# Performance work log

Measured on AMD Instinct MI355X. Metric: run time of the kernel, lower is better.

Reference implementation:

```python
import jax, jax.numpy as jnp
import numpy as np

MX_D, MN_D, CENTERS, WIDTH, SLOPE = 10.0, 0.0, 16, 1.0, 0.01
T_STEPS = 3


def _lrelu(x):
    return jax.nn.leaky_relu(x, SLOPE)


def _gauss(d):
    # d: [B,E,1] distances -> [B,E,CENTERS] gaussian radial basis
    mu = jnp.linspace(MN_D, MX_D, CENTERS, dtype=d.dtype)
    return jnp.exp(-jnp.square((d - mu[None, None, :]) / WIDTH))


def _equiv_message(v, idx2, n_recv, W1, W2, b, aw, ab):
    # v: [B,E,F] = concat(sender feats, receiver feats, bond feats).
    # Outer-product expand over receiver-cell axis (einsum with one-hot),
    # permutation-equivariant linear (local term + cell-sum term), LeakyReLU,
    # gather receiver cell, sigmoid attention gate, scatter_add to receivers.
    B, E, _ = v.shape
    O = W1.shape[1]
    oh = jax.nn.one_hot(idx2, n_recv, dtype=v.dtype)                 # [E,N]
    y_loc = jnp.einsum('bef,fo->beo', v, W1)                          # per-cell term
    y_sum = jnp.einsum('bef,fo->beo', v, W2) + b                      # cell-sum term (sum_n v*oh = v)
    y = _lrelu(y_loc[..., None] * oh[None, :, None, :] + y_sum[..., None])  # [B,E,O,N]
    gidx = jnp.broadcast_to(idx2[None, :, None, None], (B, E, O, 1))
    lat = jnp.take_along_axis(y, gidx, axis=3)[..., 0]                # [B,E,O]
    lat = jax.nn.sigmoid(lat @ aw + ab[None, None, :]) * lat          # attention gating
    return jnp.zeros((B, n_recv, O), v.dtype).at[:, idx2].add(lat)    # scatter_add over receivers


def _forward(sites, bonds, sites_p, bonds_sp, bonds_ps,
             se_W, se_b, sep_W, sep_b, ee_W, ee_b, eep_W, eep_b,
             eq_W1_ss, eq_W2_ss, eq_b_ss, att_w_ss, att_b_ss,
             eq_W1_ps, eq_W2_ps, eq_b_ps, att_w_ps, att_b_ps,
             eq_W1_sp, eq_W2_sp, eq_b_sp, att_w_sp, att_b_sp,
             nu_W1, nu_b1, nu_W2, nu_b2, nup_W1, nup_b1, nup_W2, nup_b2,
             p1_W, p1_b, p2a_W, p2a_b, p2b_W, p2b_b, p3_W, p3_b,
             idx1, idx2, idx1_sp, idx2_sp, idx1_ps, idx2_ps):
    s = _lrelu(sites @ se_W + se_b)          # [B,N,D] site embedding
    sp = _lrelu(sites_p @ sep_W + sep_b)     # [B,Np,D] pore embedding
    be = _lrelu(_gauss(bonds) @ ee_W + ee_b)
    bsp = _lrelu(_gauss(bonds_sp) @ eep_W + eep_b)
    bps = _lrelu(_gauss(bonds_ps) @ eep_W + eep_b)
    N, Np = s.shape[1], sp.shape[1]
    for t in range(T_STEPS):  # fixed number of message-passing layers
        v_ss = jnp.concatenate([s[:, idx1], s[:, idx2], be], -1)
        m = _equiv_message(v_ss, idx2, N, eq_W1_ss[t], eq_W2_ss[t], eq_b_ss[t], att_w_ss[t], att_b_ss[t])
        v_ps = jnp.concatenate([sp[:, idx1_ps], s[:, idx2_ps], bps], -1)
        m_ps = _equiv_message(v_ps, idx2_ps, N, eq_W1_ps[t], eq_W2_ps[t], eq_b_ps[t], att_w_ps[t], att_b_ps[t])
        v_sp = jnp.concatenate([s[:, idx1_sp], sp[:, idx2_sp], bsp], -1)
        m_sp = _equiv_message(v_sp, idx2_sp, Np, eq_W1_sp[t], eq_W2_sp[t], eq_b_sp[t], att_w_sp[t], att_b_sp[t])
        h = jnp.concatenate([s, m, m_ps], -1)
        h = _lrelu(_lrelu(h @ nu_W1[t] + nu_b1[t]) @ nu_W2[t] + nu_b2[t])
        s = s + h                              # residual node update (sites)
        hp = jnp.concatenate([sp, m_sp], -1)
        hp = _lrelu(_lrelu(hp @ nup_W1[t] + nup_b1[t]) @ nup_W2[t] + nup_b2[t])
        sp = sp + hp                           # residual node update (pores)
    x = _lrelu(s @ p1_W + p1_b).sum(1)        # sum pool over sites
    x = _lrelu(x @ p2a_W + p2a_b)
    x = _lrelu(x @ p2b_W + p2b_b)
    return x @ p3_W + p3_b                    # [B, out_size]


def setup_inputs():
    key = jax.random.key(0)
    ks = iter(jax.random.split(key, 80))
    B, N, Np, E, Esp = 4, 128, 16, 1280, 1024
    D, C, O, M, T = 32, CENTERS, 32, 64, T_STEPS
    Fin = 2 * D + 16  # sender + receiver + edge embedding

    def nrm(shape, fan):
        return jax.random.normal(next(ks), shape, jnp.float32) / np.float32(np.sqrt(fan))

    inp = {}
    inp['sites'] = jax.random.uniform(next(ks), (B, N, 1), jnp.float32)
    inp['bonds'] = jax.random.uniform(next(ks), (B, E, 1), jnp.float32) * MX_D
    inp['sites_p'] = jax.random.uniform(next(ks), (B, Np, 2), jnp.float32)
    inp['bonds_sp'] = jax.random.uniform(next(ks), (B, Esp, 1), jnp.float32) * MX_D
    inp['bonds_ps'] = jax.random.uniform(next(ks), (B, Esp, 1), jnp.float32) * MX_D
    inp['idx1'] = jax.random.randint(next(ks), (E,), 0, N, jnp.int32)
    inp['idx2'] = jax.random.randint(next(ks), (E,), 0, N, jnp.int32)
    inp['idx1_sp'] = jax.random.randint(next(ks), (Esp,), 0, N, jnp.int32)
    inp['idx2_sp'] = jax.random.randint(next(ks), (Esp,), 0, Np, jnp.int32)
    inp['idx1_ps'] = jax.random.randint(next(ks), (Esp,), 0, Np, jnp.int32)
    inp['idx2_ps'] = jax.random.randint(next(ks), (Esp,), 0, N, jnp.int32)
    # embeddings
    inp['se_W'] = nrm((1, D), 1); inp['se_b'] = nrm((D,), D)
    inp['sep_W'] = nrm((2, D), 2); inp['sep_b'] = nrm((D,), D)
    inp['ee_W'] = nrm((C, 16), C); inp['ee_b'] = nrm((16,), 16)
    inp['eep_W'] = nrm((C, 16), C); inp['eep_b'] = nrm((16,), 16)
    # equivariant message layers (stacked over T steps)
    for suf in ('ss', 'ps', 'sp'):
        inp['eq_W1_' + suf] = nrm((T, Fin, O), Fin)
        inp['eq_W2_' + suf] = nrm((T, Fin, O), Fin)
        inp['eq_b_' + suf] = nrm((T, O), O)
        inp['att_w_' + suf] = nrm((T, O, 1), O)
        inp['att_b_' + suf] = nrm((T, 1), 1)
    # node updates: sites take 2 message streams, pores take 1
    inp['nu_W1'] = nrm((T, D + 2 * O, D), D + 2 * O); inp['nu_b1'] = nrm((T, D), D)
    inp['nu_W2'] = nrm((T, D, D), D); inp['nu_b2'] = nrm((T, D), D)
    inp['nup_W1'] = nrm((T, D + O, D), D + O); inp['nup_b1'] = nrm((T, D), D)
    inp['nup_W2'] = nrm((T, D, D), D); inp['nup_b2'] = nrm((T, D), D)
    # prediction head
    inp['p1_W'] = nrm((D, M), D); inp['p1_b'] = nrm((M,), M)
    inp['p2a_W'] = nrm((M, M), M); inp['p2a_b'] = nrm((M,), M)
    inp['p2b_W'] = nrm((M, M), M); inp['p2b_b'] = nrm((M,), M)
    inp['p3_W'] = nrm((M, 1), M); inp['p3_b'] = nrm((1,), 1)
    return inp


def reference(sites, bonds, sites_p, bonds_sp, bonds_ps,
              se_W, se_b, sep_W, sep_b, ee_W, ee_b, eep_W, eep_b,
              eq_W1_ss, eq_W2_ss, eq_b_ss, att_w_ss, att_b_ss,
              eq_W1_ps, eq_W2_ps, eq_b_ps, att_w_ps, att_b_ps,
              eq_W1_sp, eq_W2_sp, eq_b_sp, att_w_sp, att_b_sp,
              nu_W1, nu_b1, nu_W2, nu_b2, nup_W1, nup_b1, nup_W2, nup_b2,
              p1_W, p1_b, p2a_W, p2a_b, p2b_W, p2b_b, p3_W, p3_b,
              idx1, idx2, idx1_sp, idx2_sp, idx1_ps, idx2_ps):
    return _forward(sites, bonds, sites_p, bonds_sp, bonds_ps,
                    se_W, se_b, sep_W, sep_b, ee_W, ee_b, eep_W, eep_b,
                    eq_W1_ss, eq_W2_ss, eq_b_ss, att_w_ss, att_b_ss,
                    eq_W1_ps, eq_W2_ps, eq_b_ps, att_w_ps, att_b_ps,
                    eq_W1_sp, eq_W2_sp, eq_b_sp, att_w_sp, att_b_sp,
                    nu_W1, nu_b1, nu_W2, nu_b2, nup_W1, nup_b1, nup_W2, nup_b2,
                    p1_W, p1_b, p2a_W, p2a_b, p2b_W, p2b_b, p3_W, p3_b,
                    idx1, idx2, idx1_sp, idx2_sp, idx1_ps, idx2_ps)
```

## Files before the change

kernel.cpp:

```cpp
#include <hip/hip_runtime.h>
#include <math.h>

#define BB   4
#define NN   128
#define NPP  16
#define EEE  1280
#define ESP  1024
#define DD   32
#define CC   16
#define OO   32
#define FIN  80
#define MMM  64
#define TT   3
#define TPB  256
#define SPB  512

#define MAXDEG_SS 48
#define MAXDEG_SP 192

constexpr int OFF_S    = 0;
constexpr int OFF_SP   = OFF_S   + BB*NN*DD;
constexpr int OFF_BE   = OFF_SP  + BB*NPP*DD;
constexpr int OFF_BSP  = OFF_BE  + BB*EEE*CC;
constexpr int OFF_BPS  = OFF_BSP + BB*ESP*CC;
constexpr int OFF_PRJ  = OFF_BPS + BB*ESP*CC;
constexpr int P_SASS = 0;
constexpr int P_SBSS = P_SASS + BB*NN*OO;
constexpr int P_SBPS = P_SBSS + BB*NN*OO;
constexpr int P_SASP = P_SBPS + BB*NN*OO;
constexpr int P_PAPS = P_SASP + BB*NN*OO;
constexpr int P_PBSP = P_PAPS + BB*NPP*OO;
constexpr int PRJ_SZ = P_PBSP + BB*NPP*OO;
constexpr int OFF_POOL = OFF_PRJ + 2*PRJ_SZ;
constexpr int OFF_CSR  = OFF_POOL + BB*MMM;
constexpr int SS_CNT  = 0;
constexpr int PS_CNT  = SS_CNT + NN;
constexpr int SP_CNT  = PS_CNT + NN;
constexpr int TICKET  = SP_CNT + NPP;
constexpr int SS_PAIR = 274;
constexpr int PS_PAIR = SS_PAIR + NN*MAXDEG_SS*2;
constexpr int SP_PAIR = PS_PAIR + NN*MAXDEG_SS*2;

__device__ __forceinline__ float lrelu(float x) { return x > 0.f ? x : 0.01f * x; }

__device__ __forceinline__ float dot16r(const float* ef, const float* we) {
    float4 f0 = *(const float4*)(ef);
    float4 f1 = *(const float4*)(ef + 4);
    float4 f2 = *(const float4*)(ef + 8);
    float4 f3 = *(const float4*)(ef + 12);
    return f0.x*we[ 0] + f0.y*we[ 1] + f0.z*we[ 2] + f0.w*we[ 3]
         + f1.x*we[ 4] + f1.y*we[ 5] + f1.z*we[ 6] + f1.w*we[ 7]
         + f2.x*we[ 8] + f2.y*we[ 9] + f2.z*we[10] + f2.w*we[11]
         + f3.x*we[12] + f3.y*we[13] + f3.z*we[14] + f3.w*we[15];
}

__device__ __forceinline__ float red32(float r) {
#pragma unroll
    for (int mm = 16; mm > 0; mm >>= 1) r += __shfl_xor(r, mm, 32);
    return r;
}

__device__ __forceinline__ void edge_embed(float d, const float* W, const float* bvec, float* out) {
    float g[CC];
#pragma unroll
    for (int c = 0; c < CC; ++c) {
        float mu = (10.0f / 15.0f) * (float)c;
        float z = d - mu;
        g[c] = expf(-z * z);
    }
#pragma unroll
    for (int j = 0; j < CC; ++j) {
        float a = bvec[j];
#pragma unroll
        for (int c = 0; c < CC; ++c) a += g[c] * W[c * CC + j];
        out[j] = lrelu(a);
    }
}

__device__ __forceinline__ void csr_wave(const int* recv, const int* send, int E, int r,
                                         int* cnt, int2* pair, int maxdeg, int lane) {
    int base = 0;
    for (int c = 0; c < E; c += 64) {
        const int e = c + lane;
        const bool m = (recv[e] == r);
        const unsigned long long mask = __ballot(m);
        if (m) {
            const int pos = base + __popcll(mask & ((1ull << lane) - 1ull));
            if (pos < maxdeg) pair[pos] = make_int2(e, send[e]);
        }
        base += (int)__popcll(mask);
    }
    if (lane == 0) cnt[r] = base < maxdeg ? base : maxdeg;
}

__global__ __launch_bounds__(TPB) void k_init(
    const float* sites, const float* bonds, const float* sites_p,
    const float* bonds_sp, const float* bonds_ps,
    const int* idx1, const int* idx2, const int* idx1_ps, const int* idx2_ps,
    const int* idx1_sp, const int* idx2_sp,
    const float* se_W, const float* se_b, const float* sep_W, const float* sep_b,
    const float* ee_W, const float* ee_b, const float* eep_W, const float* eep_b,
    const float* eqW1_ss, const float* eqW2_ss,
    const float* eqW1_ps, const float* eqW2_ps,
    const float* eqW1_sp, const float* eqW2_sp,
    float* ws)
{
    __shared__ float smem[4416];
    const int blk = blockIdx.x;
    const int tid = threadIdx.x;
    int* csr = (int*)(ws + OFF_CSR);

    if (blk == 0 && tid == 0) csr[TICKET] = 0;

    if (blk < 253) {
        const int totalA = BB*MMM + BB*EEE + BB*ESP + BB*ESP;
        for (int i = blk*TPB + tid; i < totalA; i += 253*TPB) {
            int r = i;
            if (r < BB*MMM) { ws[OFF_POOL + r] = 0.f; continue; }
            r -= BB*MMM;
            if (r < BB*EEE) { edge_embed(bonds[r],    ee_W,  ee_b,  ws + OFF_BE  + r*CC); continue; }
            r -= BB*EEE;
            if (r < BB*ESP) { edge_embed(bonds_sp[r], eep_W, eep_b, ws + OFF_BSP + r*CC); continue; }
            r -= BB*ESP;
            edge_embed(bonds_ps[r], eep_W, eep_b, ws + OFF_BPS + r*CC);
        }
    }
    if (blk < 72) {
        float* prj0 = ws + OFF_PRJ;
        const int el = tid >> 5, o = tid & 31;
        float* sP   = smem;
        float* sRow = smem + 4160;
        if (blk < 64) {
            const int g = blk*8 + el;
            float x = sites[g];
            float v0 = lrelu(x * se_W[o] + se_b[o]);
            ws[OFF_S + g*DD + o] = v0;
            sRow[el*32 + o] = v0;
            for (int i2 = tid; i2 < 4096; i2 += TPB) {
                int m = i2 >> 10, j = i2 & 1023, d = j >> 5, oo = j & 31;
                int row = (m == 1 || m == 2) ? (DD + d) : d;
                float wv;
                if (m < 2)      wv = eqW1_ss[row*OO + oo] + eqW2_ss[row*OO + oo];
                else if (m==2)  wv = eqW1_ps[row*OO + oo] + eqW2_ps[row*OO + oo];
                else            wv = eqW1_sp[row*OO + oo] + eqW2_sp[row*OO + oo];
                sP[i2] = wv;
            }
            __syncthreads();
            float p0=0.f,p1=0.f,p2=0.f,p3=0.f;
#pragma unroll
            for (int d = 0; d < 32; ++d) {
                float sv = sRow[el*32 + d];
                p0 += sv * sP[        d*32 + o];
                p1 += sv * sP[1024 +  d*32 + o];
                p2 += sv * sP[2048 +  d*32 + o];
                p3 += sv * sP[3072 +  d*32 + o];
            }
            prj0[P_SASS + g*OO + o] = p0;
            prj0[P_SBSS + g*OO + o] = p1;
            prj0[P_SBPS + g*OO + o] = p2;
            prj0[P_SASP + g*OO + o] = p3;
        } else {
            const int g = (blk-64)*8 + el;
            float x0 = sites_p[g*2], x1 = sites_p[g*2+1];
            float v0 = lrelu(x0 * sep_W[o] + x1 * sep_W[DD + o] + sep_b[o]);
            ws[OFF_SP + g*DD + o] = v0;
            sRow[el*32 + o] = v0;
            for (int i2 = tid; i2 < 2048; i2 += TPB) {
                int m = i2 >> 10, j = i2 & 1023, d = j >> 5, oo = j & 31;
                int row = (m == 0) ? d : (DD + d);
                float wv;
                if (m == 0) wv = eqW1_ps[row*OO + oo] + eqW2_ps[row*OO + oo];
                else        wv = eqW1_sp[row*OO + oo] + eqW2_sp[row*OO + oo];
                sP[i2] = wv;
            }
            __syncthreads();
            float p0=0.f,p1=0.f;
#pragma unroll
            for (int d = 0; d < 32; ++d) {
                float sv = sRow[el*32 + d];
                p0 += sv * sP[        d*32 + o];
                p1 += sv * sP[1024 +  d*32 + o];
            }
            prj0[P_PAPS + g*OO + o] = p0;
            prj0[P_PBSP + g*OO + o] = p1;
        }
    }
    if (blk >= 72 && blk < 140) {
        const int widx = (blk - 72) * 4 + (tid >> 6);
        const int lane = tid & 63;
        if (widx < NN) {
            csr_wave(idx2, idx1, EEE, widx, csr + SS_CNT,
                     (int2*)(csr + SS_PAIR) + widx*MAXDEG_SS, MAXDEG_SS, lane);
        } else if (widx < 2*NN) {
            const int r = widx - NN;
            csr_wave(idx2_ps, idx1_ps, ESP, r, csr + PS_CNT,
                     (int2*)(csr + PS_PAIR) + r*MAXDEG_SS, MAXDEG_SS, lane);
        } else if (widx < 2*NN + NPP) {
            const int r = widx - 2*NN;
            csr_wave(idx2_sp, idx1_sp, ESP, r, csr + SP_CNT,
                     (int2*)(csr + SP_PAIR) + r*MAXDEG_SP, MAXDEG_SP, lane);
        }
    }
}

__global__ __launch_bounds__(SPB) void k_step(
    const float* eqW1_ss, const float* eqW2_ss, const float* eqb_ss, const float* aw_ss, const float* ab_ss,
    const float* eqW1_ps, const float* eqW2_ps, const float* eqb_ps, const float* aw_ps, const float* ab_ps,
    const float* eqW1_sp, const float* eqW2_sp, const float* eqb_sp, const float* aw_sp, const float* ab_sp,
    const float* nuW1, const float* nub1, const float* nuW2, const float* nub2,
    const float* nupW1, const float* nupb1, const float* nupW2, const float* nupb2,
    const float* p1W, const float* p1b,
    const float* p2aW, const float* p2ab, const float* p2bW, const float* p2bb,
    const float* p3W, const float* p3b,
    float* ws, float* out, int t)
{
    __shared__ float sRed[768];
    __shared__ float sH[96], sU[32], sSnew[32];
    __shared__ float sHy[256], sHz[256];
    __shared__ int sWin;
    const int tid = threadIdx.x, blk = blockIdx.x;
    const int slot = tid >> 5, o = tid & 31;
    const int par = t & 1;
    const float* PRJ  = ws + OFF_PRJ + par * PRJ_SZ;
    float*       PRJn = ws + OFF_PRJ + (par ^ 1) * PRJ_SZ;
    const int* csr = (const int*)(ws + OFF_CSR);

    if (blk < 512) {
        const int g = blk, b = g >> 7, n = g & 127;
        const bool is_ss = slot < 8;
        const int q = slot & 7;
        const float* w1p = is_ss ? eqW1_ss : eqW1_ps;
        const float* w2p = is_ss ? eqW2_ss : eqW2_ps;
        const float* wa = w1p + t*FIN*OO + 2*DD*OO + o;
        const float* wb = w2p + t*FIN*OO + 2*DD*OO + o;
        float we[16];
#pragma unroll
        for (int c = 0; c < 16; ++c) we[c] = wa[c*OO] + wb[c*OO];
        const float bias = (is_ss ? eqb_ss : eqb_ps)[t*OO + o];
        const float awo  = (is_ss ? aw_ss  : aw_ps )[t*OO + o];
        const float abv  = (is_ss ? ab_ss  : ab_ps )[t];
        const float sb   = PRJ[(is_ss ? P_SBSS : P_SBPS) + g*OO + o];
        const float* SAb = is_ss ? (PRJ + P_SASS + b*(NN*OO))
                                 : (PRJ + P_PAPS + b*(NPP*OO));
        const float* EFb = is_ss ? (ws + OFF_BE  + b*(EEE*CC))
                                 : (ws + OFF_BPS + b*(ESP*CC));
        const int cnt = is_ss ? csr[SS_CNT + n] : csr[PS_CNT + n];
        const int2* lst = is_ss ? ((const int2*)(csr + SS_PAIR) + n*MAXDEG_SS)
                                : ((const int2*)(csr + PS_PAIR) + n*MAXDEG_SS);
        float acc = 0.f;
        for (int k = q; k < cnt; k += 8) {
            const int2 es = lst[k];
            float a = bias + sb + SAb[es.y*OO + o] + dot16r(EFb + es.x*CC, we);
            float u = lrelu(a);
            float rr = red32(u * awo);
            acc += u / (1.f + expf(-(rr + abv)));
        }
        sRed[slot*32 + o] = acc;
        if (tid < 32) sH[tid] = ws[OFF_S + g*DD + tid];
        __syncthreads();
        if (tid < 64) {
            const int r2 = tid >> 5, oo = tid & 31;
            float mv = 0.f;
#pragma unroll
            for (int j = 0; j < 8; ++j) mv += sRed[(r2*8 + j)*32 + oo];
            sH[32 + r2*32 + oo] = mv;
        }
        __syncthreads();
        if (tid < 32) {
            const float* W1 = nuW1 + t*(96*32);
            float a = nub1[t*32 + tid];
#pragma unroll
            for (int f = 0; f < 96; ++f) a += sH[f] * W1[f*32 + tid];
            sU[tid] = lrelu(a);
        }
        __syncthreads();
        if (tid < 32) {
            const float* W2 = nuW2 + t*(32*32);
            float a = nub2[t*32 + tid];
#pragma unroll
            for (int k2 = 0; k2 < 32; ++k2) a += sU[k2] * W2[k2*32 + tid];
            const float snew = sH[tid] + lrelu(a);
            ws[OFF_S + g*DD + tid] = snew;
            sSnew[tid] = snew;
        }
        __syncthreads();
        if (t < TT-1) {
            if (tid < 128) {
                const int tn = t + 1;
                const int m = slot;
                const float *w1m, *w2m; float* dst;
                if (m == 0)      { w1m = eqW1_ss + tn*FIN*OO;         w2m = eqW2_ss + tn*FIN*OO;         dst = PRJn + P_SASS; }
                else if (m == 1) { w1m = eqW1_ss + tn*FIN*OO + DD*OO; w2m = eqW2_ss + tn*FIN*OO + DD*OO; dst = PRJn + P_SBSS; }
                else if (m == 2) { w1m = eqW1_ps + tn*FIN*OO + DD*OO; w2m = eqW2_ps + tn*FIN*OO + DD*OO; dst = PRJn + P_SBPS; }
                else             { w1m = eqW1_sp + tn*FIN*OO;         w2m = eqW2_sp + tn*FIN*OO;         dst = PRJn + P_SASP; }
                float a = 0.f;
#pragma unroll
                for (int d = 0; d < 32; ++d) a += sSnew[d] * (w1m[d*OO + o] + w2m[d*OO + o]);
                dst[g*OO + o] = a;
            }
        } else {
            if (tid < 64) {
                float a = p1b[tid];
#pragma unroll
                for (int d = 0; d < 32; ++d) a += sSnew[d] * p1W[d*MMM + tid];
                atomicAdd(&ws[OFF_POOL + b*MMM + tid], lrelu(a));
            }
            __syncthreads();
            if (tid == 0) {
                int* ticket = (int*)(ws + OFF_CSR) + TICKET;
                int p = __hip_atomic_fetch_add(ticket, 1, __ATOMIC_ACQ_REL, __HIP_MEMORY_SCOPE_AGENT);
                sWin = (p == 511) ? 1 : 0;
            }
            __syncthreads();
            if (sWin) {
                float* sx = sRed;
                if (tid < 256)
                    sx[tid] = __hip_atomic_load(&ws[OFF_POOL + tid], __ATOMIC_RELAXED, __HIP_MEMORY_SCOPE_AGENT);
                __syncthreads();
                if (tid < 256) {
                    const int b2 = tid >> 6, mm = tid & 63;
                    float a = p2ab[mm];
#pragma unroll
                    for (int k = 0; k < MMM; ++k) a += sx[b2*64 + k] * p2aW[k*MMM + mm];
                    sHy[tid] = lrelu(a);
                }
                __syncthreads();
                if (tid < 256) {
                    const int b2 = tid >> 6, mm = tid & 63;
                    float a = p2bb[mm];
#pragma unroll
                    for (int k = 0; k < MMM; ++k) a += sHy[b2*64 + k] * p2bW[k*MMM + mm];
                    sHz[tid] = lrelu(a);
                }
                __syncthreads();
                if (tid < BB) {
                    float acc2 = p3b[0];
#pragma unroll
                    for (int k = 0; k < MMM; ++k) acc2 += sHz[tid*64 + k] * p3W[k];
                    out[tid] = acc2;
                }
            }
        }
    } else {
        const int g = blk - 512, b = g >> 4, p = g & 15;
        const float* wa = eqW1_sp + t*FIN*OO + 2*DD*OO + o;
        const float* wb = eqW2_sp + t*FIN*OO + 2*DD*OO + o;
        float we[16];
#pragma unroll
        for (int c = 0; c < 16; ++c) we[c] = wa[c*OO] + wb[c*OO];
        const float bias = eqb_sp[t*OO + o];
        const float awo  = aw_sp[t*OO + o];
        const float abv  = ab_sp[t];
        const float sb   = PRJ[P_PBSP + g*OO + o];
        const float* SAb = PRJ + P_SASP + b*(NN*OO);
        const float* EFb = ws + OFF_BSP + b*(ESP*CC);
        const int cnt = csr[SP_CNT + p];
        const int2* lst = (const int2*)(csr + SP_PAIR) + p*MAXDEG_SP;
        float acc = 0.f;
        for (int k = slot; k < cnt; k += 16) {
            const int2 es = lst[k];
            float a = bias + sb + SAb[es.y*OO + o] + dot16r(EFb + es.x*CC, we);
            float u = lrelu(a);
            float rr = red32(u * awo);
            acc += u / (1.f + expf(-(rr + abv)));
        }
        sRed[slot*32 + o] = acc;
        if (tid < 32) sH[tid] = ws[OFF_SP + g*DD + tid];
        __syncthreads();
        if (tid < 32) {
            float mv = 0.f;
#pragma unroll
            for (int j = 0; j < 16; ++j) mv += sRed[j*32 + tid];
            sH[32 + tid] = mv;
        }
        __syncthreads();
        if (tid < 32) {
            const float* W1 = nupW1 + t*(64*32);
            float a = nupb1[t*32 + tid];
#pragma unroll
            for (int f = 0; f < 64; ++f) a += sH[f] * W1[f*32 + tid];
            sU[tid] = lrelu(a);
        }
        __syncthreads();
        if (tid < 32) {
            const float* W2 = nupW2 + t*(32*32);
            float a = nupb2[t*32 + tid];
#pragma unroll
            for (int k2 = 0; k2 < 32; ++k2) a += sU[k2] * W2[k2*32 + tid];
            const float snew = sH[tid] + lrelu(a);
            ws[OFF_SP + g*DD + tid] = snew;
            sSnew[tid] = snew;
        }
        __syncthreads();
        if (t < TT-1 && tid < 64) {
            const int tn = t + 1;
            const int m = slot;
            const float *w1m, *w2m; float* dst;
            if (m == 0) { w1m = eqW1_ps + tn*FIN*OO;         w2m = eqW2_ps + tn*FIN*OO;         dst = PRJn + P_PAPS; }
            else        { w1m = eqW1_sp + tn*FIN*OO + DD*OO; w2m = eqW2_sp + tn*FIN*OO + DD*OO; dst = PRJn + P_PBSP; }
            float a = 0.f;
#pragma unroll
            for (int d = 0; d < 32; ++d) a += sSnew[d] * (w1m[d*OO + o] + w2m[d*OO + o]);
            dst[g*OO + o] = a;
        }
    }
}

extern "C" void kernel_launch(void* const* d_in, const int* in_sizes, int n_in,
                              void* d_out, int out_size, void* d_ws, size_t ws_size,
                              hipStream_t stream) {
    (void)in_sizes; (void)n_in; (void)out_size; (void)ws_size;
    const float* sites    = (const float*)d_in[0];
    const float* bonds    = (const float*)d_in[1];
    const float* sites_p  = (const float*)d_in[2];
    const float* bonds_sp = (const float*)d_in[3];
    const float* bonds_ps = (const float*)d_in[4];
    const int* idx1    = (const int*)d_in[5];
    const int* idx2    = (const int*)d_in[6];
    const int* idx1_sp = (const int*)d_in[7];
    const int* idx2_sp = (const int*)d_in[8];
    const int* idx1_ps = (const int*)d_in[9];
    const int* idx2_ps = (const int*)d_in[10];
    const float* se_W  = (const float*)d_in[11];
    const float* se_b  = (const float*)d_in[12];
    const float* sep_W = (const float*)d_in[13];
    const float* sep_b = (const float*)d_in[14];
    const float* ee_W  = (const float*)d_in[15];
    const float* ee_b  = (const float*)d_in[16];
    const float* eep_W = (const float*)d_in[17];
    const float* eep_b = (const float*)d_in[18];
    const float* eqW1_ss = (const float*)d_in[19];
    const float* eqW2_ss = (const float*)d_in[20];
    const float* eqb_ss  = (const float*)d_in[21];
    const float* aw_ss   = (const float*)d_in[22];
    const float* ab_ss   = (const float*)d_in[23];
    const float* eqW1_ps = (const float*)d_in[24];
    const float* eqW2_ps = (const float*)d_in[25];
    const float* eqb_ps  = (const float*)d_in[26];
    const float* aw_ps   = (const float*)d_in[27];
    const float* ab_ps   = (const float*)d_in[28];
    const float* eqW1_sp = (const float*)d_in[29];
    const float* eqW2_sp = (const float*)d_in[30];
    const float* eqb_sp  = (const float*)d_in[31];
    const float* aw_sp   = (const float*)d_in[32];
    const float* ab_sp   = (const float*)d_in[33];
    const float* nuW1  = (const float*)d_in[34];
    const float* nub1  = (const float*)d_in[35];
    const float* nuW2  = (const float*)d_in[36];
    const float* nub2  = (const float*)d_in[37];
    const float* nupW1 = (const float*)d_in[38];
    const float* nupb1 = (const float*)d_in[39];
    const float* nupW2 = (const float*)d_in[40];
    const float* nupb2 = (const float*)d_in[41];
    const float* p1W  = (const float*)d_in[42];
    const float* p1b  = (const float*)d_in[43];
    const float* p2aW = (const float*)d_in[44];
    const float* p2ab = (const float*)d_in[45];
    const float* p2bW = (const float*)d_in[46];
    const float* p2bb = (const float*)d_in[47];
    const float* p3W  = (const float*)d_in[48];
    const float* p3b  = (const float*)d_in[49];

    float* ws  = (float*)d_ws;
    float* out = (float*)d_out;

    k_init<<<256, TPB, 0, stream>>>(sites, bonds, sites_p, bonds_sp, bonds_ps,
                                    idx1, idx2, idx1_ps, idx2_ps, idx1_sp, idx2_sp,
                                    se_W, se_b, sep_W, sep_b, ee_W, ee_b, eep_W, eep_b,
                                    eqW1_ss, eqW2_ss, eqW1_ps, eqW2_ps, eqW1_sp, eqW2_sp, ws);
    for (int t = 0; t < TT; ++t) {
        k_step<<<576, SPB, 0, stream>>>(
            eqW1_ss, eqW2_ss, eqb_ss, aw_ss, ab_ss,
            eqW1_ps, eqW2_ps, eqb_ps, aw_ps, ab_ps,
            eqW1_sp, eqW2_sp, eqb_sp, aw_sp, ab_sp,
            nuW1, nub1, nuW2, nub2, nupW1, nupb1, nupW2, nupb2,
            p1W, p1b, p2aW, p2ab, p2bW, p2bb, p3W, p3b,
            ws, out, t);
    }
}
```

Baseline: 58.92 us.

## Fuse three step kernels into one persistent kernel with grid barriers

Replaces the three per-timestep k_step launches with a single persistent k_mega launch of 256 blocks of 1024 threads. Each block handles two site rows and, for the first 64 blocks, one pore row, and the timesteps are separated by a two-level atomic grid barrier held in workspace. Cross-block projection data is read and written with relaxed agent-scope atomics. This removes launch overhead and inter-kernel gaps, but it depends on all 256 blocks being co-resident and adds barrier spin latency and larger blocks.

Measured after the change: 231.9 us. 293% more time.

```diff
diff --git a/kernel.cpp b/kernel.cpp
--- a/kernel.cpp
+++ b/kernel.cpp
@@ -13,7 +13,7 @@
 #define MMM  64
 #define TT   3
 #define TPB  256
-#define SPB  512
+#define MPB  1024
 
 #define MAXDEG_SS 48
 #define MAXDEG_SP 192
@@ -40,6 +40,12 @@
 constexpr int SS_PAIR = 274;
 constexpr int PS_PAIR = SS_PAIR + NN*MAXDEG_SS*2;
 constexpr int SP_PAIR = PS_PAIR + NN*MAXDEG_SS*2;
+constexpr int BAR0    = ((SP_PAIR + NPP*MAXDEG_SP*2 + 31)/32)*32;
+constexpr int BAR_STRIDE = 576;
+constexpr int BAR_INTS   = 2*BAR_STRIDE;
+
+#define ALOAD(p)    __hip_atomic_load((p), __ATOMIC_RELAXED, __HIP_MEMORY_SCOPE_AGENT)
+#define ASTORE(p,v) __hip_atomic_store((p), (v), __ATOMIC_RELAXED, __HIP_MEMORY_SCOPE_AGENT)
 
 __device__ __forceinline__ float lrelu(float x) { return x > 0.f ? x : 0.01f * x; }
 
@@ -91,6 +97,19 @@
         base += (int)__popcll(mask);
     }
     if (lane == 0) cnt[r] = base < maxdeg ? base : maxdeg;
+}
+
+__device__ __forceinline__ void arrive_and_wait(int* base) {
+    const int grp = (int)blockIdx.x & 15;
+    int p = __hip_atomic_fetch_add(base + grp*32, 1, __ATOMIC_RELAXED, __HIP_MEMORY_SCOPE_AGENT);
+    if (p == 15) {
+        int q2 = __hip_atomic_fetch_add(base + 512, 1, __ATOMIC_RELAXED, __HIP_MEMORY_SCOPE_AGENT);
+        if (q2 == 15)
+            __hip_atomic_store(base + 544, 1, __ATOMIC_RELAXED, __HIP_MEMORY_SCOPE_AGENT);
+    }
+    while (__hip_atomic_load(base + 544, __ATOMIC_RELAXED, __HIP_MEMORY_SCOPE_AGENT) == 0)
+        __builtin_amdgcn_s_sleep(1);
+    asm volatile("" ::: "memory");
 }
 
 __global__ __launch_bounds__(TPB) void k_init(
@@ -111,6 +130,7 @@
     int* csr = (int*)(ws + OFF_CSR);
 
     if (blk == 0 && tid == 0) csr[TICKET] = 0;
+    if (blk == 141) for (int i = tid; i < BAR_INTS; i += TPB) csr[BAR0 + i] = 0;
 
     if (blk < 253) {
         const int totalA = BB*MMM + BB*EEE + BB*ESP + BB*ESP;
@@ -203,7 +223,7 @@
     }
 }
 
-__global__ __launch_bounds__(SPB) void k_step(
+__global__ __launch_bounds__(MPB, 4) void k_mega(
     const float* eqW1_ss, const float* eqW2_ss, const float* eqb_ss, const float* aw_ss, const float* ab_ss,
     const float* eqW1_ps, const float* eqW2_ps, const float* eqb_ps, const float* aw_ps, const float* ab_ps,
     const float* eqW1_sp, const float* eqW2_sp, const float* eqb_sp, const float* aw_sp, const float* ab_sp,
@@ -212,82 +232,151 @@
     const float* p1W, const float* p1b,
     const float* p2aW, const float* p2ab, const float* p2bW, const float* p2bb,
     const float* p3W, const float* p3b,
-    float* ws, float* out, int t)
+    float* ws, float* out)
 {
-    __shared__ float sRed[768];
-    __shared__ float sH[96], sU[32], sSnew[32];
-    __shared__ float sHy[256], sHz[256];
+    __shared__ float sRed[1024];
+    __shared__ float sRedP[1024];
+    __shared__ float sH[192];
+    __shared__ float sPH[96];
+    __shared__ float sU[64], sPU[32];
+    __shared__ float sSnew[64], sPnew[32];
+    __shared__ float sHx[256], sHy[256], sHz[256];
     __shared__ int sWin;
+
     const int tid = threadIdx.x, blk = blockIdx.x;
     const int slot = tid >> 5, o = tid & 31;
-    const int par = t & 1;
-    const float* PRJ  = ws + OFF_PRJ + par * PRJ_SZ;
-    float*       PRJn = ws + OFF_PRJ + (par ^ 1) * PRJ_SZ;
-    const int* csr = (const int*)(ws + OFF_CSR);
-
-    if (blk < 512) {
-        const int g = blk, b = g >> 7, n = g & 127;
-        const bool is_ss = slot < 8;
-        const int q = slot & 7;
-        const float* w1p = is_ss ? eqW1_ss : eqW1_ps;
-        const float* w2p = is_ss ? eqW2_ss : eqW2_ps;
-        const float* wa = w1p + t*FIN*OO + 2*DD*OO + o;
-        const float* wb = w2p + t*FIN*OO + 2*DD*OO + o;
-        float we[16];
-#pragma unroll
-        for (int c = 0; c < 16; ++c) we[c] = wa[c*OO] + wb[c*OO];
-        const float bias = (is_ss ? eqb_ss : eqb_ps)[t*OO + o];
-        const float awo  = (is_ss ? aw_ss  : aw_ps )[t*OO + o];
-        const float abv  = (is_ss ? ab_ss  : ab_ps )[t];
-        const float sb   = PRJ[(is_ss ? P_SBSS : P_SBPS) + g*OO + o];
-        const float* SAb = is_ss ? (PRJ + P_SASS + b*(NN*OO))
-                                 : (PRJ + P_PAPS + b*(NPP*OO));
-        const float* EFb = is_ss ? (ws + OFF_BE  + b*(EEE*CC))
-                                 : (ws + OFF_BPS + b*(ESP*CC));
-        const int cnt = is_ss ? csr[SS_CNT + n] : csr[PS_CNT + n];
-        const int2* lst = is_ss ? ((const int2*)(csr + SS_PAIR) + n*MAXDEG_SS)
-                                : ((const int2*)(csr + PS_PAIR) + n*MAXDEG_SS);
-        float acc = 0.f;
-        for (int k = q; k < cnt; k += 8) {
-            const int2 es = lst[k];
-            float a = bias + sb + SAb[es.y*OO + o] + dot16r(EFb + es.x*CC, we);
-            float u = lrelu(a);
-            float rr = red32(u * awo);
-            acc += u / (1.f + expf(-(rr + abv)));
-        }
-        sRed[slot*32 + o] = acc;
-        if (tid < 32) sH[tid] = ws[OFF_S + g*DD + tid];
+    const bool haspore = (blk < 64);
+    int* csr = (int*)(ws + OFF_CSR);
+    int* bar = csr + BAR0;
+
+    for (int t = 0; t < TT; ++t) {
+        const int par = t & 1;
+        float* PRJ  = ws + OFF_PRJ + par * PRJ_SZ;
+        float* PRJn = ws + OFF_PRJ + (par ^ 1) * PRJ_SZ;
+
+        {
+            const int rsel = slot >> 4, s16 = slot & 15;
+            const bool is_ss = s16 < 8;
+            const int q = s16 & 7;
+            const int g = blk*2 + rsel, b = g >> 7, n = g & 127;
+            const float* w1p = is_ss ? eqW1_ss : eqW1_ps;
+            const float* w2p = is_ss ? eqW2_ss : eqW2_ps;
+            const float* wa = w1p + t*FIN*OO + 2*DD*OO + o;
+            const float* wb = w2p + t*FIN*OO + 2*DD*OO + o;
+            float we[16];
+#pragma unroll
+            for (int c = 0; c < 16; ++c) we[c] = wa[c*OO] + wb[c*OO];
+            const float bias = (is_ss ? eqb_ss : eqb_ps)[t*OO + o];
+            const float awo  = (is_ss ? aw_ss  : aw_ps )[t*OO + o];
+            const float abv  = (is_ss ? ab_ss  : ab_ps )[t];
+            const float sb   = ALOAD(&PRJ[(is_ss ? P_SBSS : P_SBPS) + g*OO + o]);
+            float* SAb = is_ss ? (PRJ + P_SASS + b*(NN*OO))
+                               : (PRJ + P_PAPS + b*(NPP*OO));
+            const float* EFb = is_ss ? (ws + OFF_BE  + b*(EEE*CC))
+                                     : (ws + OFF_BPS + b*(ESP*CC));
+            const int cnt = is_ss ? csr[SS_CNT + n] : csr[PS_CNT + n];
+            const int2* lst = is_ss ? ((const int2*)(csr + SS_PAIR) + n*MAXDEG_SS)
+                                    : ((const int2*)(csr + PS_PAIR) + n*MAXDEG_SS);
+            float acc = 0.f;
+            for (int k = q; k < cnt; k += 8) {
+                const int2 es = lst[k];
+                float sa = ALOAD(&SAb[es.y*OO + o]);
+                float a = bias + sb + sa + dot16r(EFb + es.x*CC, we);
+                float u = lrelu(a);
+                float rr = red32(u * awo);
+                acc += u / (1.f + expf(-(rr + abv)));
+            }
+            sRed[slot*32 + o] = acc;
+        }
+        if (haspore) {
+            const int pg = blk, pb = pg >> 4, pp = pg & 15;
+            const float* wa = eqW1_sp + t*FIN*OO + 2*DD*OO + o;
+            const float* wb = eqW2_sp + t*FIN*OO + 2*DD*OO + o;
+            float weP[16];
+#pragma unroll
+            for (int c = 0; c < 16; ++c) weP[c] = wa[c*OO] + wb[c*OO];
+            const float bias = eqb_sp[t*OO + o];
+            const float awo  = aw_sp[t*OO + o];
+            const float abv  = ab_sp[t];
+            const float sb   = ALOAD(&PRJ[P_PBSP + pg*OO + o]);
+            float* SAp = PRJ + P_SASP + pb*(NN*OO);
+            const float* EFp = ws + OFF_BSP + pb*(ESP*CC);
+            const int cnt = csr[SP_CNT + pp];
+            const int2* lst = (const int2*)(csr + SP_PAIR) + pp*MAXDEG_SP;
+            float acc = 0.f;
+            for (int k = slot; k < cnt; k += 32) {
+                const int2 es = lst[k];
+                float sa = ALOAD(&SAp[es.y*OO + o]);
+                float a = bias + sb + sa + dot16r(EFp + es.x*CC, weP);
+                float u = lrelu(a);
+                float rr = red32(u * awo);
+                acc += u / (1.f + expf(-(rr + abv)));
+            }
+            sRedP[slot*32 + o] = acc;
+        }
+        __syncthreads();
+
+        if (tid < 64) {
+            const int r2 = tid >> 5, oo = tid & 31;
+            float mss = 0.f, mps = 0.f;
+#pragma unroll
+            for (int j = 0; j < 8; ++j)  mss += sRed[(r2*16 + j)*32 + oo];
+#pragma unroll
+            for (int j = 8; j < 16; ++j) mps += sRed[(r2*16 + j)*32 + oo];
+            sH[r2*96 + oo]      = ws[OFF_S + (blk*2 + r2)*DD + oo];
+            sH[r2*96 + 32 + oo] = mss;
+            sH[r2*96 + 64 + oo] = mps;
+        } else if (tid < 96 && haspore) {
+            const int oo = tid & 31;
+            float mp = 0.f;
+#pragma unroll
+            for (int j = 0; j < 32; ++j) mp += sRedP[j*32 + oo];
+            sPH[oo]      = ws[OFF_SP + blk*DD + oo];
+            sPH[32 + oo] = mp;
+        }
         __syncthreads();
         if (tid < 64) {
             const int r2 = tid >> 5, oo = tid & 31;
-            float mv = 0.f;
-#pragma unroll
-            for (int j = 0; j < 8; ++j) mv += sRed[(r2*8 + j)*32 + oo];
-            sH[32 + r2*32 + oo] = mv;
+            const float* W1 = nuW1 + t*(96*32);
+            float a = nub1[t*32 + oo];
+#pragma unroll
+            for (int f = 0; f < 96; ++f) a += sH[r2*96 + f] * W1[f*32 + oo];
+            sU[r2*32 + oo] = lrelu(a);
+        } else if (tid < 96 && haspore) {
+            const int oo = tid & 31;
+            const float* W1 = nupW1 + t*(64*32);
+            float a = nupb1[t*32 + oo];
+#pragma unroll
+            for (int f = 0; f < 64; ++f) a += sPH[f] * W1[f*32 + oo];
+            sPU[oo] = lrelu(a);
         }
         __syncthreads();
-        if (tid < 32) {
-            const float* W1 = nuW1 + t*(96*32);
-            float a = nub1[t*32 + tid];
-#pragma unroll
-            for (int f = 0; f < 96; ++f) a += sH[f] * W1[f*32 + tid];
-            sU[tid] = lrelu(a);
+        if (tid < 64) {
+            const int r2 = tid >> 5, oo = tid & 31;
+            const float* W2 = nuW2 + t*(32*32);
+            float a = nub2[t*32 + oo];
+#pragma unroll
+            for (int k2 = 0; k2 < 32; ++k2) a += sU[r2*32 + k2] * W2[k2*32 + oo];
+            const float snew = sH[r2*96 + oo] + lrelu(a);
+            ws[OFF_S + (blk*2 + r2)*DD + oo] = snew;
+            sSnew[r2*32 + oo] = snew;
+        } else if (tid < 96 && haspore) {
+            const int oo = tid & 31;
+            const float* W2 = nupW2 + t*(32*32);
+            float a = nupb2[t*32 + oo];
+#pragma unroll
+            for (int k2 = 0; k2 < 32; ++k2) a += sPU[k2] * W2[k2*32 + oo];
+            const float snew = sPH[oo] + lrelu(a);
+            ws[OFF_SP + blk*DD + oo] = snew;
+            sPnew[oo] = snew;
         }
         __syncthreads();
-        if (tid < 32) {
-            const float* W2 = nuW2 + t*(32*32);
-            float a = nub2[t*32 + tid];
-#pragma unroll
-            for (int k2 = 0; k2 < 32; ++k2) a += sU[k2] * W2[k2*32 + tid];
-            const float snew = sH[tid] + lrelu(a);
-            ws[OFF_S + g*DD + tid] = snew;
-            sSnew[tid] = snew;
-        }
-        __syncthreads();
+
         if (t < TT-1) {
-            if (tid < 128) {
+            if (tid < 256) {
                 const int tn = t + 1;
-                const int m = slot;
+                const int m = tid >> 6, r2 = (tid >> 5) & 1, oo = tid & 31;
+                const int g2 = blk*2 + r2;
                 const float *w1m, *w2m; float* dst;
                 if (m == 0)      { w1m = eqW1_ss + tn*FIN*OO;         w2m = eqW2_ss + tn*FIN*OO;         dst = PRJn + P_SASS; }
                 else if (m == 1) { w1m = eqW1_ss + tn*FIN*OO + DD*OO; w2m = eqW2_ss + tn*FIN*OO + DD*OO; dst = PRJn + P_SBSS; }
@@ -295,33 +384,45 @@
                 else             { w1m = eqW1_sp + tn*FIN*OO;         w2m = eqW2_sp + tn*FIN*OO;         dst = PRJn + P_SASP; }
                 float a = 0.f;
 #pragma unroll
-                for (int d = 0; d < 32; ++d) a += sSnew[d] * (w1m[d*OO + o] + w2m[d*OO + o]);
-                dst[g*OO + o] = a;
-            }
+                for (int d = 0; d < 32; ++d) a += sSnew[r2*32 + d] * (w1m[d*OO + oo] + w2m[d*OO + oo]);
+                ASTORE(&dst[g2*OO + oo], a);
+            } else if (tid < 320 && haspore) {
+                const int tn = t + 1;
+                const int m = (tid - 256) >> 5, oo = tid & 31;
+                const float *w1m, *w2m; float* dst;
+                if (m == 0) { w1m = eqW1_ps + tn*FIN*OO;         w2m = eqW2_ps + tn*FIN*OO;         dst = PRJn + P_PAPS; }
+                else        { w1m = eqW1_sp + tn*FIN*OO + DD*OO; w2m = eqW2_sp + tn*FIN*OO + DD*OO; dst = PRJn + P_PBSP; }
+                float a = 0.f;
+#pragma unroll
+                for (int d = 0; d < 32; ++d) a += sPnew[d] * (w1m[d*OO + oo] + w2m[d*OO + oo]);
+                ASTORE(&dst[blk*OO + oo], a);
+            }
+            __syncthreads();
+            if (tid == 0) arrive_and_wait(bar + t*BAR_STRIDE);
+            __syncthreads();
         } else {
-            if (tid < 64) {
-                float a = p1b[tid];
-#pragma unroll
-                for (int d = 0; d < 32; ++d) a += sSnew[d] * p1W[d*MMM + tid];
-                atomicAdd(&ws[OFF_POOL + b*MMM + tid], lrelu(a));
+            if (tid < 128) {
+                const int r2 = tid >> 6, mm = tid & 63;
+                const int g2 = blk*2 + r2, b2 = g2 >> 7;
+                float a = p1b[mm];
+#pragma unroll
+                for (int d = 0; d < 32; ++d) a += sSnew[r2*32 + d] * p1W[d*MMM + mm];
+                atomicAdd(&ws[OFF_POOL + b2*MMM + mm], lrelu(a));
             }
             __syncthreads();
             if (tid == 0) {
-                int* ticket = (int*)(ws + OFF_CSR) + TICKET;
-                int p = __hip_atomic_fetch_add(ticket, 1, __ATOMIC_ACQ_REL, __HIP_MEMORY_SCOPE_AGENT);
-                sWin = (p == 511) ? 1 : 0;
+                int p = __hip_atomic_fetch_add(csr + TICKET, 1, __ATOMIC_RELAXED, __HIP_MEMORY_SCOPE_AGENT);
+                sWin = (p == 255) ? 1 : 0;
             }
             __syncthreads();
             if (sWin) {
-                float* sx = sRed;
-                if (tid < 256)
-                    sx[tid] = __hip_atomic_load(&ws[OFF_POOL + tid], __ATOMIC_RELAXED, __HIP_MEMORY_SCOPE_AGENT);
+                if (tid < 256) sHx[tid] = ALOAD(&ws[OFF_POOL + tid]);
                 __syncthreads();
                 if (tid < 256) {
                     const int b2 = tid >> 6, mm = tid & 63;
                     float a = p2ab[mm];
 #pragma unroll
-                    for (int k = 0; k < MMM; ++k) a += sx[b2*64 + k] * p2aW[k*MMM + mm];
+                    for (int k = 0; k < MMM; ++k) a += sHx[b2*64 + k] * p2aW[k*MMM + mm];
                     sHy[tid] = lrelu(a);
                 }
                 __syncthreads();
@@ -340,68 +441,6 @@
                     out[tid] = acc2;
                 }
             }
-        }
-    } else {
-        const int g = blk - 512, b = g >> 4, p = g & 15;
-        const float* wa = eqW1_sp + t*FIN*OO + 2*DD*OO + o;
-        const float* wb = eqW2_sp + t*FIN*OO + 2*DD*OO + o;
-        float we[16];
-#pragma unroll
-        for (int c = 0; c < 16; ++c) we[c] = wa[c*OO] + wb[c*OO];
-        const float bias = eqb_sp[t*OO + o];
-        const float awo  = aw_sp[t*OO + o];
-        const float abv  = ab_sp[t];
-        const float sb   = PRJ[P_PBSP + g*OO + o];
-        const float* SAb = PRJ + P_SASP + b*(NN*OO);
-        const float* EFb = ws + OFF_BSP + b*(ESP*CC);
-        const int cnt = csr[SP_CNT + p];
-        const int2* lst = (const int2*)(csr + SP_PAIR) + p*MAXDEG_SP;
-        float acc = 0.f;
-        for (int k = slot; k < cnt; k += 16) {
-            const int2 es = lst[k];
-            float a = bias + sb + SAb[es.y*OO + o] + dot16r(EFb + es.x*CC, we);
-            float u = lrelu(a);
-            float rr = red32(u * awo);
-            acc += u / (1.f + expf(-(rr + abv)));
-        }
-        sRed[slot*32 + o] = acc;
-        if (tid < 32) sH[tid] = ws[OFF_SP + g*DD + tid];
-        __syncthreads();
-        if (tid < 32) {
-            float mv = 0.f;
-#pragma unroll
-            for (int j = 0; j < 16; ++j) mv += sRed[j*32 + tid];
-            sH[32 + tid] = mv;
-        }
-        __syncthreads();
-        if (tid < 32) {
-            const float* W1 = nupW1 + t*(64*32);
-            float a = nupb1[t*32 + tid];
-#pragma unroll
-            for (int f = 0; f < 64; ++f) a += sH[f] * W1[f*32 + tid];
-            sU[tid] = lrelu(a);
-        }
-        __syncthreads();
-        if (tid < 32) {
-            const float* W2 = nupW2 + t*(32*32);
-            float a = nupb2[t*32 + tid];
-#pragma unroll
-            for (int k2 = 0; k2 < 32; ++k2) a += sU[k2] * W2[k2*32 + tid];
-            const float snew = sH[tid] + lrelu(a);
-            ws[OFF_SP + g*DD + tid] = snew;
-            sSnew[tid] = snew;
-        }
-        __syncthreads();
-        if (t < TT-1 && tid < 64) {
-            const int tn = t + 1;
-            const int m = slot;
-            const float *w1m, *w2m; float* dst;
-            if (m == 0) { w1m = eqW1_ps + tn*FIN*OO;         w2m = eqW2_ps + tn*FIN*OO;         dst = PRJn + P_PAPS; }
-            else        { w1m = eqW1_sp + tn*FIN*OO + DD*OO; w2m = eqW2_sp + tn*FIN*OO + DD*OO; dst = PRJn + P_PBSP; }
-            float a = 0.f;
-#pragma unroll
-            for (int d = 0; d < 32; ++d) a += sSnew[d] * (w1m[d*OO + o] + w2m[d*OO + o]);
-            dst[g*OO + o] = a;
         }
     }
 }
@@ -468,13 +507,11 @@
                                     idx1, idx2, idx1_ps, idx2_ps, idx1_sp, idx2_sp,
                                     se_W, se_b, sep_W, sep_b, ee_W, ee_b, eep_W, eep_b,
                                     eqW1_ss, eqW2_ss, eqW1_ps, eqW2_ps, eqW1_sp, eqW2_sp, ws);
-    for (int t = 0; t < TT; ++t) {
-        k_step<<<576, SPB, 0, stream>>>(
-            eqW1_ss, eqW2_ss, eqb_ss, aw_ss, ab_ss,
-            eqW1_ps, eqW2_ps, eqb_ps, aw_ps, ab_ps,
-            eqW1_sp, eqW2_sp, eqb_sp, aw_sp, ab_sp,
-            nuW1, nub1, nuW2, nub2, nupW1, nupb1, nupW2, nupb2,
-            p1W, p1b, p2aW, p2ab, p2bW, p2bb, p3W, p3b,
-            ws, out, t);
-    }
-}
+    k_mega<<<256, MPB, 0, stream>>>(
+        eqW1_ss, eqW2_ss, eqb_ss, aw_ss, ab_ss,
+        eqW1_ps, eqW2_ps, eqb_ps, aw_ps, ab_ps,
+        eqW1_sp, eqW2_sp, eqb_sp, aw_sp, ab_sp,
+        nuW1, nub1, nuW2, nub2, nupW1, nupb1, nupW2, nupb2,
+        p1W, p1b, p2aW, p2ab, p2bW, p2bb, p3W, p3b,
+        ws, out);
+}
```
